# Performance work log

Hardware: AMD Instinct MI355X
Metric: run time of the kernel (lower is better)

Reference implementation:

```python
import jax, jax.numpy as jnp
import numpy as np

K = 1024
D = 64
BETA = 0.25


def setup_inputs() -> dict:
    key = jax.random.key(0)
    k1, k2 = jax.random.split(key)
    latents = jax.random.normal(k1, (32, 64, 64, 64), dtype=jnp.float32)  # [B, C=D, H, W]
    # embedding init: uniform(-1/K, 1/K)
    embedding = jax.random.uniform(k2, (K, D), dtype=jnp.float32, minval=-1.0 / K, maxval=1.0 / K)
    return {"latents": latents, "embedding": embedding}


def reference(latents, embedding):
    # [B, D, H, W] -> [B, H, W, D]
    x = jnp.transpose(latents, (0, 2, 3, 1))
    shp = x.shape
    flat = x.reshape(-1, D)  # [N, D]

    dist = (jnp.sum(flat ** 2, axis=1, keepdims=True)
            + jnp.sum(embedding ** 2, axis=1)
            - 2.0 * flat @ embedding.T)  # [N, K]
    inds = jnp.argmin(dist, axis=1)  # [N]

    quantized = embedding[inds].reshape(shp)  # gather == one-hot @ embedding

    commitment_loss = jnp.mean((jax.lax.stop_gradient(quantized) - x) ** 2)
    embedding_loss = jnp.mean((quantized - jax.lax.stop_gradient(x)) ** 2)
    vq_loss = commitment_loss * BETA + embedding_loss

    # straight-through estimator
    quantized = x + jax.lax.stop_gradient(quantized - x)
    out = jnp.transpose(quantized, (0, 3, 1, 2))  # back to [B, D, H, W]
    return out, vq_loss
```

## Files before the change

### kernel.cpp

```cpp
#include <hip/hip_runtime.h>
#include <hip/hip_bf16.h>


#define HW 4096
#define OUTELEMS 8388608

typedef __attribute__((ext_vector_type(8))) short bf16x8;
typedef __attribute__((ext_vector_type(4))) float f32x4;
typedef __attribute__((ext_vector_type(4))) int i32x4;

static __device__ __forceinline__ short f2bf(float f) {
    union { __hip_bfloat16 h; short s; } u;
    u.h = __float2bfloat16(f);
    return u.s;
}
static __device__ __forceinline__ unsigned umin2(unsigned a, unsigned b) {
    return a < b ? a : b;
}


__global__ __launch_bounds__(256) void prep_kernel(const float* __restrict__ emb,
                                                   short* __restrict__ Ebf,
                                                   float* __restrict__ en1,
                                                   float* __restrict__ loss) {
    int code = blockIdx.x * 4 + (threadIdx.x >> 6);
    int d = threadIdx.x & 63;
    float v = emb[code * 64 + d];
    int g = d >> 3, j = d & 7;
    Ebf[code * 64 + ((g + code) & 7) * 8 + j] = f2bf(-2.0f * v);
    float s = v * v;
#pragma unroll
    for (int off = 32; off > 0; off >>= 1) s += __shfl_xor(s, off, 64);
    if (d == 0) en1[code] = 1.0f + s;
    if (blockIdx.x == 0 && threadIdx.x == 0) *loss = 0.0f;
}

__global__ __launch_bounds__(1024, 4) void vq_kernel(
        const float* __restrict__ lat, const short* __restrict__ Ebf,
        const float* __restrict__ en1, float* __restrict__ out,
        float* __restrict__ loss) {
    extern __shared__ __align__(16) char sbuf[];
    const int tid  = threadIdx.x;
    const int wave = tid >> 6;
    const int lane = tid & 63;
    const int n    = lane & 15;
    const int quad = lane >> 4;

    const int g0 = blockIdx.x * 512;
    const int b  = g0 >> 12;
    const int mb = g0 & 4095;
    const float* latb = lat + (size_t)b * 262144;

    {
        const f32x4* src = (const f32x4*)Ebf;
        f32x4* dst = (f32x4*)sbuf;
#pragma unroll
        for (int r = 0; r < 8; ++r)
            dst[r * 1024 + tid] = src[r * 1024 + tid];
        if (tid < 256)
            ((f32x4*)(sbuf + 131072))[tid] = ((const f32x4*)en1)[tid];
    }

    bf16x8 bfr[2][2];
    float xnorm[2];
#pragma unroll
    for (int s = 0; s < 2; ++s) {
        const float* xp = latb + (mb + wave * 32 + s * 16 + n);
        float xs = 0.0f; bf16x8 f0, f1;
#pragma unroll
        for (int j = 0; j < 8; ++j) {
            float x0 = xp[(quad * 8 + j) * HW];
            float x1 = xp[(32 + quad * 8 + j) * HW];
            xs += x0 * x0 + x1 * x1;
            f0[j] = f2bf(x0); f1[j] = f2bf(x1);
        }
        bfr[s][0] = f0; bfr[s][1] = f1; xnorm[s] = xs;
    }
    __syncthreads();

    const int slot0 = ((quad + n) & 7) * 16;
    const int slot1 = ((quad + 4 + n) & 7) * 16;
    const char* arowBase = sbuf + n * 128;
    const f32x4* enl = (const f32x4*)(sbuf + 131072);
    unsigned emin[2] = {0xFFFFFFFFu, 0xFFFFFFFFu};

#pragma unroll 2
    for (int ct = 0; ct < 64; ++ct) {
        const char* rb = arowBase + ct * 2048;
        bf16x8 a0 = *(const bf16x8*)(rb + slot0);
        bf16x8 a1 = *(const bf16x8*)(rb + slot1);
        f32x4 en4 = enl[ct * 4 + quad];
        f32x4 acc0 = __builtin_amdgcn_mfma_f32_16x16x32_bf16(a0, bfr[0][0], en4, 0, 0, 0);
        f32x4 acc1 = __builtin_amdgcn_mfma_f32_16x16x32_bf16(a0, bfr[1][0], en4, 0, 0, 0);
        acc0 = __builtin_amdgcn_mfma_f32_16x16x32_bf16(a1, bfr[0][1], acc0, 0, 0, 0);
        acc1 = __builtin_amdgcn_mfma_f32_16x16x32_bf16(a1, bfr[1][1], acc1, 0, 0, 0);
        const unsigned cb = ct * 16 + quad * 4;
        unsigned e0 = (__float_as_uint(acc0[0]) & 0xFFFFFC00u) | (cb + 0);
        unsigned e1 = (__float_as_uint(acc0[1]) & 0xFFFFFC00u) | (cb + 1);
        unsigned e2 = (__float_as_uint(acc0[2]) & 0xFFFFFC00u) | (cb + 2);
        unsigned e3 = (__float_as_uint(acc0[3]) & 0xFFFFFC00u) | (cb + 3);
        emin[0] = umin2(emin[0], umin2(umin2(e0, e1), umin2(e2, e3)));
        unsigned f0 = (__float_as_uint(acc1[0]) & 0xFFFFFC00u) | (cb + 0);
        unsigned f1 = (__float_as_uint(acc1[1]) & 0xFFFFFC00u) | (cb + 1);
        unsigned f2 = (__float_as_uint(acc1[2]) & 0xFFFFFC00u) | (cb + 2);
        unsigned f3 = (__float_as_uint(acc1[3]) & 0xFFFFFC00u) | (cb + 3);
        emin[1] = umin2(emin[1], umin2(umin2(f0, f1), umin2(f2, f3)));
    }

#pragma unroll
    for (int off = 16; off <= 32; off <<= 1) {
#pragma unroll
        for (int s = 0; s < 2; ++s) {
            unsigned eo = (unsigned)__shfl_xor((int)emin[s], off, 64);
            float xo = __shfl_xor(xnorm[s], off, 64);
            emin[s] = eo < emin[s] ? eo : emin[s];
            xnorm[s] += xo;
        }
    }

    int* codes = (int*)(sbuf + 135168);
    if (quad == 0) {
        codes[wave * 32 + n]      = (int)(emin[0] & 1023u);
        codes[wave * 32 + 16 + n] = (int)(emin[1] & 1023u);
    }

    float contrib = 0.0f;
#pragma unroll
    for (int s = 0; s < 2; ++s)
        contrib += __uint_as_float(emin[s] & 0xFFFFFC00u) - 1.0f + xnorm[s];
#pragma unroll
    for (int off = 32; off > 0; off >>= 1) contrib += __shfl_xor(contrib, off, 64);
    float* wsum = (float*)(sbuf + 137216);
    if (lane == 0) wsum[wave] = contrib;
    __syncthreads();
    if (tid == 0) {
        float t = 0.0f;
#pragma unroll
        for (int w = 0; w < 16; ++w) t += wsum[w];
        atomicAdd(loss, t * (1.25f / (8388608.0f * 4.0f)));
    }

    float* outb = out + (size_t)b * 262144 + mb;
#pragma unroll 2
    for (int i = 0; i < 8; ++i) {
        int id = i * 1024 + tid;
        int d  = id >> 7;
        int mq = (id & 127) * 4;
        i32x4 c4 = *(const i32x4*)(codes + mq);
        int g = d >> 3, j2 = (d & 7) * 2;
        unsigned u0 = *(const unsigned short*)(sbuf + c4.x * 128 + ((g + c4.x) & 7) * 16 + j2);
        unsigned u1 = *(const unsigned short*)(sbuf + c4.y * 128 + ((g + c4.y) & 7) * 16 + j2);
        unsigned u2 = *(const unsigned short*)(sbuf + c4.z * 128 + ((g + c4.z) & 7) * 16 + j2);
        unsigned u3 = *(const unsigned short*)(sbuf + c4.w * 128 + ((g + c4.w) & 7) * 16 + j2);
        f32x4 v;
        v[0] = __uint_as_float(u0 << 16) * -0.5f;
        v[1] = __uint_as_float(u1 << 16) * -0.5f;
        v[2] = __uint_as_float(u2 << 16) * -0.5f;
        v[3] = __uint_as_float(u3 << 16) * -0.5f;
        *(f32x4*)(outb + d * HW + mq) = v;
    }
}

extern "C" void kernel_launch(void* const* d_in, const int* in_sizes, int n_in,
                              void* d_out, int out_size, void* d_ws, size_t ws_size,
                              hipStream_t stream) {
    const float* latents   = (const float*)d_in[0];
    const float* embedding = (const float*)d_in[1];
    float* out  = (float*)d_out;
    float* loss = out + OUTELEMS;

    char* ws = (char*)d_ws;
    short* Ebf = (short*)ws;
    float* en1 = (float*)(ws + 131072);

    hipFuncSetAttribute((const void*)vq_kernel,
                        hipFuncAttributeMaxDynamicSharedMemorySize, 137280);

    prep_kernel<<<256, 256, 0, stream>>>(embedding, Ebf, en1, loss);
    vq_kernel<<<256, 1024, 137280, stream>>>(latents, Ebf, en1, out, loss);
}
```

Measured before the change: 106.2 us.

## Halve block size, give each wave four query tiles, prefetch codebook fragments

Blocks drop from 1024 to 512 threads, and each wave now handles 64 latent positions (four 16-row tiles) instead of 32. Each codebook fragment read from LDS is therefore reused across four MFMA chains, which halves LDS read traffic per MFMA. The next iteration's codebook fragments and norms are loaded one step ahead, so LDS latency overlaps the MFMAs. The cost is higher register pressure and half as many waves per block to hide the global latency of the loads and stores.

```diff
diff --git a/kernel.cpp b/kernel.cpp
--- a/kernel.cpp
+++ b/kernel.cpp
@@ -35,7 +35,7 @@
     if (blockIdx.x == 0 && threadIdx.x == 0) *loss = 0.0f;
 }
 
-__global__ __launch_bounds__(1024, 4) void vq_kernel(
+__global__ __launch_bounds__(512, 2) void vq_kernel(
         const float* __restrict__ lat, const short* __restrict__ Ebf,
         const float* __restrict__ en1, float* __restrict__ out,
         float* __restrict__ loss) {
@@ -55,17 +55,17 @@
         const f32x4* src = (const f32x4*)Ebf;
         f32x4* dst = (f32x4*)sbuf;
 #pragma unroll
-        for (int r = 0; r < 8; ++r)
-            dst[r * 1024 + tid] = src[r * 1024 + tid];
+        for (int r = 0; r < 16; ++r)
+            dst[r * 512 + tid] = src[r * 512 + tid];
         if (tid < 256)
             ((f32x4*)(sbuf + 131072))[tid] = ((const f32x4*)en1)[tid];
     }
 
-    bf16x8 bfr[2][2];
-    float xnorm[2];
+    bf16x8 bfr[4][2];
+    float xnorm[4];
 #pragma unroll
-    for (int s = 0; s < 2; ++s) {
-        const float* xp = latb + (mb + wave * 32 + s * 16 + n);
+    for (int s = 0; s < 4; ++s) {
+        const float* xp = latb + (mb + wave * 64 + s * 16 + n);
         float xs = 0.0f; bf16x8 f0, f1;
 #pragma unroll
         for (int j = 0; j < 8; ++j) {
@@ -82,35 +82,44 @@
     const int slot1 = ((quad + 4 + n) & 7) * 16;
     const char* arowBase = sbuf + n * 128;
     const f32x4* enl = (const f32x4*)(sbuf + 131072);
-    unsigned emin[2] = {0xFFFFFFFFu, 0xFFFFFFFFu};
+    unsigned emin[4] = {0xFFFFFFFFu, 0xFFFFFFFFu, 0xFFFFFFFFu, 0xFFFFFFFFu};
 
-#pragma unroll 2
+    bf16x8 a0 = *(const bf16x8*)(arowBase + slot0);
+    bf16x8 a1 = *(const bf16x8*)(arowBase + slot1);
+    f32x4 en4 = enl[quad];
+
+#pragma unroll 4
     for (int ct = 0; ct < 64; ++ct) {
-        const char* rb = arowBase + ct * 2048;
-        bf16x8 a0 = *(const bf16x8*)(rb + slot0);
-        bf16x8 a1 = *(const bf16x8*)(rb + slot1);
-        f32x4 en4 = enl[ct * 4 + quad];
-        f32x4 acc0 = __builtin_amdgcn_mfma_f32_16x16x32_bf16(a0, bfr[0][0], en4, 0, 0, 0);
-        f32x4 acc1 = __builtin_amdgcn_mfma_f32_16x16x32_bf16(a0, bfr[1][0], en4, 0, 0, 0);
-        acc0 = __builtin_amdgcn_mfma_f32_16x16x32_bf16(a1, bfr[0][1], acc0, 0, 0, 0);
-        acc1 = __builtin_amdgcn_mfma_f32_16x16x32_bf16(a1, bfr[1][1], acc1, 0, 0, 0);
+        const int nx = (ct + 1) & 63;
+        const char* rb = arowBase + nx * 2048;
+        bf16x8 na0 = *(const bf16x8*)(rb + slot0);
+        bf16x8 na1 = *(const bf16x8*)(rb + slot1);
+        f32x4 nen = enl[nx * 4 + quad];
+
+        f32x4 acc[4];
+#pragma unroll
+        for (int s = 0; s < 4; ++s)
+            acc[s] = __builtin_amdgcn_mfma_f32_16x16x32_bf16(a0, bfr[s][0], en4, 0, 0, 0);
+#pragma unroll
+        for (int s = 0; s < 4; ++s)
+            acc[s] = __builtin_amdgcn_mfma_f32_16x16x32_bf16(a1, bfr[s][1], acc[s], 0, 0, 0);
+
         const unsigned cb = ct * 16 + quad * 4;
-        unsigned e0 = (__float_as_uint(acc0[0]) & 0xFFFFFC00u) | (cb + 0);
-        unsigned e1 = (__float_as_uint(acc0[1]) & 0xFFFFFC00u) | (cb + 1);
-        unsigned e2 = (__float_as_uint(acc0[2]) & 0xFFFFFC00u) | (cb + 2);
-        unsigned e3 = (__float_as_uint(acc0[3]) & 0xFFFFFC00u) | (cb + 3);
-        emin[0] = umin2(emin[0], umin2(umin2(e0, e1), umin2(e2, e3)));
-        unsigned f0 = (__float_as_uint(acc1[0]) & 0xFFFFFC00u) | (cb + 0);
-        unsigned f1 = (__float_as_uint(acc1[1]) & 0xFFFFFC00u) | (cb + 1);
-        unsigned f2 = (__float_as_uint(acc1[2]) & 0xFFFFFC00u) | (cb + 2);
-        unsigned f3 = (__float_as_uint(acc1[3]) & 0xFFFFFC00u) | (cb + 3);
-        emin[1] = umin2(emin[1], umin2(umin2(f0, f1), umin2(f2, f3)));
+#pragma unroll
+        for (int s = 0; s < 4; ++s) {
+            unsigned e0 = (__float_as_uint(acc[s][0]) & 0xFFFFFC00u) | (cb + 0);
+            unsigned e1 = (__float_as_uint(acc[s][1]) & 0xFFFFFC00u) | (cb + 1);
+            unsigned e2 = (__float_as_uint(acc[s][2]) & 0xFFFFFC00u) | (cb + 2);
+            unsigned e3 = (__float_as_uint(acc[s][3]) & 0xFFFFFC00u) | (cb + 3);
+            emin[s] = umin2(umin2(umin2(e0, e1), umin2(e2, e3)), emin[s]);
+        }
+        a0 = na0; a1 = na1; en4 = nen;
     }
 
 #pragma unroll
     for (int off = 16; off <= 32; off <<= 1) {
 #pragma unroll
-        for (int s = 0; s < 2; ++s) {
+        for (int s = 0; s < 4; ++s) {
             unsigned eo = (unsigned)__shfl_xor((int)emin[s], off, 64);
             float xo = __shfl_xor(xnorm[s], off, 64);
             emin[s] = eo < emin[s] ? eo : emin[s];
@@ -120,13 +129,14 @@
 
     int* codes = (int*)(sbuf + 135168);
     if (quad == 0) {
-        codes[wave * 32 + n]      = (int)(emin[0] & 1023u);
-        codes[wave * 32 + 16 + n] = (int)(emin[1] & 1023u);
+#pragma unroll
+        for (int s = 0; s < 4; ++s)
+            codes[wave * 64 + s * 16 + n] = (int)(emin[s] & 1023u);
     }
 
     float contrib = 0.0f;
 #pragma unroll
-    for (int s = 0; s < 2; ++s)
+    for (int s = 0; s < 4; ++s)
         contrib += __uint_as_float(emin[s] & 0xFFFFFC00u) - 1.0f + xnorm[s];
 #pragma unroll
     for (int off = 32; off > 0; off >>= 1) contrib += __shfl_xor(contrib, off, 64);
@@ -136,14 +146,14 @@
     if (tid == 0) {
         float t = 0.0f;
 #pragma unroll
-        for (int w = 0; w < 16; ++w) t += wsum[w];
+        for (int w = 0; w < 8; ++w) t += wsum[w];
         atomicAdd(loss, t * (1.25f / (8388608.0f * 4.0f)));
     }
 
     float* outb = out + (size_t)b * 262144 + mb;
-#pragma unroll 2
-    for (int i = 0; i < 8; ++i) {
-        int id = i * 1024 + tid;
+#pragma unroll 4
+    for (int i = 0; i < 16; ++i) {
+        int id = i * 512 + tid;
         int d  = id >> 7;
         int mq = (id & 127) * 4;
         i32x4 c4 = *(const i32x4*)(codes + mq);
@@ -177,5 +187,5 @@
                         hipFuncAttributeMaxDynamicSharedMemorySize, 137280);
 
     prep_kernel<<<256, 256, 0, stream>>>(embedding, Ebf, en1, loss);
-    vq_kernel<<<256, 1024, 137280, stream>>>(latents, Ebf, en1, out, loss);
+    vq_kernel<<<256, 512, 137280, stream>>>(latents, Ebf, en1, out, loss);
 }
```

Measured after the change: 107.6 us. No clear change (+1.3%).
